# Kernel optimization log

Measured on AMD Instinct MI355X. Metric: run time of the kernel, lower is better.

## Reference

```python
import jax, jax.numpy as jnp
import numpy as np
from jax import lax

LATENT = 64
NUM_EMB = 512
BETA = 0.25
DN = ('NCHW', 'OIHW', 'NCHW')


def conv(x, w, b, stride, pad):
    y = lax.conv_general_dilated(x, w, (stride, stride), [(pad, pad), (pad, pad)],
                                 dimension_numbers=DN)
    return y + b[None, :, None, None]


def tconv(x, w, b, stride, pad, opad):
    # torch ConvTranspose2d(k=3, stride, padding=pad, output_padding=opad)
    # == dilated conv with lhs_dilation=stride, padding (k-1-pad, k-1-pad+opad),
    #    spatially-flipped kernel. w is stored OIHW (out, in, kh, kw).
    k = w.shape[2]
    lo, hi = k - 1 - pad, k - 1 - pad + opad
    y = lax.conv_general_dilated(x, w[:, :, ::-1, ::-1], (1, 1), [(lo, hi), (lo, hi)],
                                 lhs_dilation=(stride, stride), dimension_numbers=DN)
    return y + b[None, :, None, None]


def vector_quantize(z, codebook):
    # z: (B, D, H, W); codebook: (K, D)
    B, D, H, W = z.shape
    flat = z.transpose(0, 2, 3, 1).reshape(-1, D)  # (BHW, D)
    d = (jnp.sum(flat ** 2, axis=1, keepdims=True)
         + jnp.sum(codebook ** 2, axis=1)
         - 2.0 * flat @ codebook.T)  # (BHW, K)
    idx = jnp.argmin(d, axis=1)
    q = codebook[idx].reshape(B, H, W, D).transpose(0, 3, 1, 2)  # (B, D, H, W)
    commitment = jnp.mean((lax.stop_gradient(q) - z) ** 2)
    codebook_loss = jnp.mean((q - lax.stop_gradient(z)) ** 2)
    loss = BETA * commitment + codebook_loss
    q_ste = z + lax.stop_gradient(q - z)  # straight-through estimator
    return q_ste, loss


def setup_inputs() -> dict:
    key = jax.random.key(0)
    ks = jax.random.split(key, 16)
    f32 = jnp.float32
    inp = {
        'x': jax.random.uniform(ks[0], (1024, 1, 50, 50), dtype=f32),
        'enc_w1': jax.random.normal(ks[1], (32, 1, 3, 3), f32) * 0.1,
        'enc_b1': jnp.zeros((32,), f32),
        'enc_w2': jax.random.normal(ks[2], (64, 32, 3, 3), f32) * 0.05,
        'enc_b2': jnp.zeros((64,), f32),
        'enc_w3': jax.random.normal(ks[3], (LATENT, 64, 1, 1), f32) * 0.1,
        'enc_b3': jnp.zeros((LATENT,), f32),
        'codebook': jax.random.uniform(ks[4], (NUM_EMB, LATENT), dtype=f32),
        'dec_w1': jax.random.normal(ks[5], (64, LATENT, 3, 3), f32) * 0.05,
        'dec_b1': jnp.zeros((64,), f32),
        'dec_w2': jax.random.normal(ks[6], (32, 64, 3, 3), f32) * 0.05,
        'dec_b2': jnp.zeros((32,), f32),
        'dec_w3': jax.random.normal(ks[7], (1, 32, 3, 3), f32) * 0.05,
        'dec_b3': jnp.zeros((1,), f32),
    }
    return inp


def reference(x, enc_w1, enc_b1, enc_w2, enc_b2, enc_w3, enc_b3, codebook,
              dec_w1, dec_b1, dec_w2, dec_b2, dec_w3, dec_b3):
    # encoder: (B,1,50,50) -> (B,LATENT,13,13)
    h = jax.nn.relu(conv(x, enc_w1, enc_b1, 2, 1))
    h = jax.nn.relu(conv(h, enc_w2, enc_b2, 2, 1))
    z = conv(h, enc_w3, enc_b3, 1, 0)
    q, vq_loss = vector_quantize(z, codebook)
    # decoder: 13 -> 25 -> 50
    h = jax.nn.relu(tconv(q, dec_w1, dec_b1, 2, 1, 0))
    h = jax.nn.relu(tconv(h, dec_w2, dec_b2, 2, 1, 1))
    x_recon = jax.nn.sigmoid(conv(h, dec_w3, dec_b3, 1, 1))
    return x_recon, vq_loss
```

## Files before the change

kernel.cpp:

```cpp
#include <hip/hip_runtime.h>
#include <math.h>


typedef __attribute__((ext_vector_type(8))) short s8v;
typedef __attribute__((ext_vector_type(4))) float f4v;
typedef __attribute__((ext_vector_type(4))) int i4v;
typedef __attribute__((ext_vector_type(4))) short s4v;
typedef __attribute__((ext_vector_type(2))) float f2v;

__device__ inline unsigned short f2bf(float f) {
    unsigned u = __builtin_bit_cast(unsigned, f);
    return (unsigned short)((u + 0x7fffu + ((u >> 16) & 1u)) >> 16);
}
__device__ inline float bf2f(unsigned short h) {
    return __builtin_bit_cast(float, ((unsigned)h) << 16);
}

__global__ __launch_bounds__(256) void k_prep_all(
        const float* __restrict__ cb,  const float* __restrict__ ew2,
        const float* __restrict__ ew3, const float* __restrict__ dw1,
        const float* __restrict__ dw2, const float* __restrict__ dw3,
        unsigned short* __restrict__ cbm, unsigned short* __restrict__ wB2n,
        unsigned short* __restrict__ wB1, unsigned short* __restrict__ wB2,
        unsigned short* __restrict__ wB3, float* __restrict__ cn,
        float* __restrict__ loss, f2v* __restrict__ wpk) {
    int i = blockIdx.x * 256 + threadIdx.x;
    if (i < 98304) {
        int j = i & 7, lane = (i >> 3) & 63;
        int kc = (i >> 9) % 6, nt = (i >> 9) / 6;
        int n = nt * 16 + (lane & 15);
        int k = kc * 32 + ((lane >> 4) << 3) + j;
        int seg = k >> 6, kk = k & 63;
        float c = cb[n * 64 + kk];
        unsigned short ch = f2bf(c);
        cbm[i] = (seg == 1) ? f2bf(c - bf2f(ch)) : ch;
    } else if (i < 153600) {
        int q = i - 98304;
        int j = q & 7, lane = (q >> 3) & 63;
        int kc = (q >> 9) % 27, nt = (q >> 9) / 27;
        int k = kc * 32 + ((lane >> 4) << 3) + j;
        int co = nt * 16 + (lane & 15);
        int part = (k < 288) ? 0 : (k < 576) ? 1 : 0;
        int kk = (k < 288) ? k : (k < 576) ? k - 288 : k - 576;
        int tap = kk >> 5, ci = kk & 31;
        float v = ew2[(co * 32 + ci) * 9 + tap];
        unsigned short hi = f2bf(v);
        wB2n[q] = part ? f2bf(v - bf2f(hi)) : hi;
    } else if (i < 219136) {
        int q = i - 153600;
        int j = q & 7, l = (q >> 3) & 63, kc = (q >> 9) & 7, nt = q >> 12;
        int n = nt * 16 + (l & 15), k = kc * 32 + (l >> 4) * 8 + j;
        int cls = n >> 6, co = n & 63, p = k >> 6, ci = k & 63;
        int jh = -1, jw = -1;
        if (cls == 0)      { if (p == 0) { jh = 1; jw = 1; } }
        else if (cls == 1) { if (p == 1) { jh = 1; jw = 0; } else if (p == 0) { jh = 1; jw = 2; } }
        else if (cls == 2) { if (p == 2) { jh = 0; jw = 1; } else if (p == 0) { jh = 2; jw = 1; } }
        else { if (p == 3) { jh = 0; jw = 0; } else if (p == 2) { jh = 0; jw = 2; }
               else if (p == 1) { jh = 2; jw = 0; } else { jh = 2; jw = 2; } }
        float v = (jh >= 0) ? dw1[((co * 64 + ci) * 3 + jh) * 3 + jw] : 0.f;
        wB1[q] = f2bf(v);
    } else if (i < 251904) {
        int q = i - 219136;
        int j = q & 7, l = (q >> 3) & 63, kc = (q >> 9) & 7, nt = q >> 12;
        int n = nt * 16 + (l & 15), k = kc * 32 + (l >> 4) * 8 + j;
        int cls = n >> 5, co = n & 31, p = k >> 6, ci = k & 63;
        int jh = -1, jw = -1;
        if (cls == 0)      { if (p == 0) { jh = 1; jw = 1; } }
        else if (cls == 1) { if (p == 1) { jh = 1; jw = 0; } else if (p == 0) { jh = 1; jw = 2; } }
        else if (cls == 2) { if (p == 2) { jh = 0; jw = 1; } else if (p == 0) { jh = 2; jw = 1; } }
        else { if (p == 3) { jh = 0; jw = 0; } else if (p == 2) { jh = 0; jw = 2; }
               else if (p == 1) { jh = 2; jw = 0; } else { jh = 2; jw = 2; } }
        float v = (jh >= 0) ? dw2[((co * 64 + ci) * 3 + jh) * 3 + jw] : 0.f;
        wB2[q] = f2bf(v);
    } else if (i < 264192) {
        int q = i - 251904;
        int j = q & 7, lane = (q >> 3) & 63;
        int kc = (q >> 9) % 6, nt = (q >> 9) / 6;
        int k = kc * 32 + ((lane >> 4) << 3) + j;
        int n = nt * 16 + (lane & 15);
        int part = (k < 64) ? 0 : (k < 128) ? 1 : 0;
        int kk = (k < 64) ? k : (k < 128) ? k - 64 : k - 128;
        float v = ew3[n * 64 + kk];
        unsigned short hi = f2bf(v);
        wB3[q] = part ? f2bf(v - bf2f(hi)) : hi;
    } else if (i < 264704) {
        int k = i - 264192;
        const float* r = cb + k * 64;
        float s = 0.f;
#pragma unroll
        for (int c = 0; c < 64; ++c) s += r[c] * r[c];
        cn[k] = s;
    } else if (i == 264704) {
        *loss = 0.f;
    } else if (i < 264849) {
        int q = i - 264705;
        int kw = q / 48, rem = q % 48, kh = rem / 16, ii = rem % 16;
        f2v w;
        w[0] = dw3[(2 * ii) * 9 + kh * 3 + kw];
        w[1] = dw3[(2 * ii + 1) * 9 + kh * 3 + kw];
        wpk[q] = w;
    }
}

__global__ __launch_bounds__(256) void k_conv1(const float* __restrict__ x,
                                               const float* __restrict__ w,
                                               const float* __restrict__ b,
                                               unsigned short* __restrict__ h1,
                                               int total) {
    __shared__ float4 wl4[72];
    float* wl = (float*)wl4;
    int tid = threadIdx.x;
    for (int t = tid; t < 288; t += 256) {
        int tap = t >> 5, co = t & 31;
        wl[t] = w[co * 9 + tap];
    }
    __syncthreads();
    int pix = blockIdx.x * 256 + tid;
    if (pix >= total) return;
    int n = pix / 625, p = pix % 625, oh = p / 25, ow = p % 25;
    const float* xp = x + (size_t)n * 2500;
    float4 a[8];
#pragma unroll
    for (int j = 0; j < 8; ++j) a[j] = ((const float4*)b)[j];
#pragma unroll
    for (int kh = 0; kh < 3; ++kh) {
        int ih = 2 * oh - 1 + kh;
        if ((unsigned)ih >= 50u) continue;
#pragma unroll
        for (int kw = 0; kw < 3; ++kw) {
            int iw = 2 * ow - 1 + kw;
            if ((unsigned)iw >= 50u) continue;
            float v = xp[ih * 50 + iw];
            int tap = kh * 3 + kw;
#pragma unroll
            for (int j = 0; j < 8; ++j) {
                float4 ww = wl4[tap * 8 + j];
                a[j].x += v * ww.x; a[j].y += v * ww.y;
                a[j].z += v * ww.z; a[j].w += v * ww.w;
            }
        }
    }
    unsigned short hi[32], lo[32];
#pragma unroll
    for (int j = 0; j < 8; ++j) {
        float vv[4] = {a[j].x, a[j].y, a[j].z, a[j].w};
#pragma unroll
        for (int e = 0; e < 4; ++e) {
            float v = fmaxf(vv[e], 0.f);
            unsigned short h = f2bf(v);
            hi[j * 4 + e] = h;
            lo[j * 4 + e] = f2bf(v - bf2f(h));
        }
    }
    i4v* op = (i4v*)(h1 + (size_t)pix * 64);
#pragma unroll
    for (int g = 0; g < 4; ++g) {
        i4v ph, pl;
#pragma unroll
        for (int e = 0; e < 4; ++e) {
            int b0 = g * 8 + e * 2;
            ph[e] = (int)((unsigned)hi[b0] | ((unsigned)hi[b0 + 1] << 16));
            pl[e] = (int)((unsigned)lo[b0] | ((unsigned)lo[b0 + 1] << 16));
        }
        op[g] = ph;
        op[4 + g] = pl;
    }
}

__global__ __launch_bounds__(256) void k_enc_m(const unsigned short* __restrict__ h1,
                                               const unsigned short* __restrict__ B2n,
                                               const unsigned short* __restrict__ B3,
                                               const float* __restrict__ b2,
                                               const float* __restrict__ b3,
                                               unsigned short* __restrict__ z, int npix) {
    __shared__ short a1[16 * 872];
    __shared__ short a2[16 * 200];
    __shared__ short czs[16 * 136];
    int tid = threadIdx.x, blk = blockIdx.x;
    {
        int m = tid >> 4, chunk = tid & 15;
        if (chunk < 9) {
            int pix = blk * 16 + m;
            i4v vh[4], vl[4];
#pragma unroll
            for (int g = 0; g < 4; ++g) {
                vh[g] = (i4v){0, 0, 0, 0};
                vl[g] = (i4v){0, 0, 0, 0};
            }
            if (pix < npix) {
                int n = pix / 169, p = pix % 169, oh = p / 13, ow = p % 13;
                int kh = chunk / 3, kw = chunk % 3;
                int ih = 2 * oh - 1 + kh, iw = 2 * ow - 1 + kw;
                if (((unsigned)ih < 25u) && ((unsigned)iw < 25u)) {
                    const i4v* ip = (const i4v*)(h1 + (((size_t)n * 25 + ih) * 25 + iw) * 64);
#pragma unroll
                    for (int g = 0; g < 4; ++g) { vh[g] = ip[g]; vl[g] = ip[4 + g]; }
                }
            }
            short* row = a1 + m * 872 + chunk * 32;
            i4v* d0 = (i4v*)row;
            i4v* d1 = (i4v*)(row + 288);
            i4v* d2 = (i4v*)(row + 576);
#pragma unroll
            for (int g = 0; g < 4; ++g) { d0[g] = vh[g]; d1[g] = vh[g]; d2[g] = vl[g]; }
        }
    }
    __syncthreads();
    int wave = tid >> 6, lane = tid & 63;
    int arow1 = (lane & 15) * 872 + (lane >> 4) * 8;
    f4v acc = (f4v){0.f, 0.f, 0.f, 0.f};
#pragma unroll
    for (int kc = 0; kc < 27; ++kc) {
        s8v a = *(const s8v*)(a1 + arow1 + kc * 32);
        s8v b = *(const s8v*)((const short*)B2n + ((size_t)((wave * 27 + kc) * 64 + lane)) * 8);
        acc = __builtin_amdgcn_mfma_f32_16x16x32_bf16(a, b, acc, 0, 0, 0);
    }
    {
        float bv = b2[wave * 16 + (lane & 15)];
        int n = wave * 16 + (lane & 15);
#pragma unroll
        for (int r = 0; r < 4; ++r) {
            int m = (lane >> 4) * 4 + r;
            float h = fmaxf(acc[r] + bv, 0.f);
            unsigned short hh = f2bf(h);
            unsigned short ll = f2bf(h - bf2f(hh));
            a2[m * 200 + n] = (short)hh;
            a2[m * 200 + 64 + n] = (short)hh;
            a2[m * 200 + 128 + n] = (short)ll;
        }
    }
    __syncthreads();
    int arow2 = (lane & 15) * 200 + (lane >> 4) * 8;
    f4v acc2 = (f4v){0.f, 0.f, 0.f, 0.f};
#pragma unroll
    for (int kc = 0; kc < 6; ++kc) {
        s8v a = *(const s8v*)(a2 + arow2 + kc * 32);
        s8v b = *(const s8v*)((const short*)B3 + ((size_t)((wave * 6 + kc) * 64 + lane)) * 8);
        acc2 = __builtin_amdgcn_mfma_f32_16x16x32_bf16(a, b, acc2, 0, 0, 0);
    }
    {
        float bv = b3[wave * 16 + (lane & 15)];
        int n = wave * 16 + (lane & 15);
#pragma unroll
        for (int r = 0; r < 4; ++r) {
            int m = (lane >> 4) * 4 + r;
            float v = acc2[r] + bv;
            unsigned short hh = f2bf(v);
            czs[m * 136 + n] = (short)hh;
            czs[m * 136 + 64 + n] = (short)f2bf(v - bf2f(hh));
        }
    }
    __syncthreads();
    {
        int m = tid >> 4, t = tid & 15;
        int pix = blk * 16 + m;
        if (pix < npix)
            *(i4v*)(z + (size_t)pix * 128 + t * 8) = *(i4v*)(czs + m * 136 + t * 8);
    }
}

__global__ __launch_bounds__(256, 2) void k_vq_m(const unsigned short* __restrict__ z,
                                                 const float* __restrict__ cb,
                                                 const unsigned short* __restrict__ cbm,
                                                 const float* __restrict__ cn,
                                                 unsigned short* __restrict__ q,
                                                 float* __restrict__ lpart, int npix) {
    __shared__ short a_lds[128 * 136];
    __shared__ int bkf[128];
    __shared__ float lred4[4];
    int tid = threadIdx.x, blk = blockIdx.x;
    {
        const i4v* src = (const i4v*)(z + (size_t)blk * 128 * 128);
#pragma unroll
        for (int it = 0; it < 8; ++it) {
            int L = it * 256 + tid;
            int m = L >> 4, s = L & 15;
            int pix = blk * 128 + m;
            i4v v = (i4v){0, 0, 0, 0};
            if (pix < npix) v = src[L];
            *(i4v*)(a_lds + m * 136 + s * 8) = v;
        }
    }
    __syncthreads();
    int wave = tid >> 6, lane = tid & 63;
    int arow0 = (wave * 32 + (lane & 15)) * 136 + (lane >> 4) * 8;
    int arow1 = arow0 + 16 * 136;
    s8v af00 = *(const s8v*)(a_lds + arow0);
    s8v af01 = *(const s8v*)(a_lds + arow0 + 32);
    s8v af02 = *(const s8v*)(a_lds + arow0 + 64);
    s8v af03 = *(const s8v*)(a_lds + arow0 + 96);
    s8v af10 = *(const s8v*)(a_lds + arow1);
    s8v af11 = *(const s8v*)(a_lds + arow1 + 32);
    s8v af12 = *(const s8v*)(a_lds + arow1 + 64);
    s8v af13 = *(const s8v*)(a_lds + arow1 + 96);
    float bd0[4], bd1[4];
    int bk0[4], bk1[4];
#pragma unroll
    for (int r = 0; r < 4; ++r) {
        bd0[r] = 3.4e38f; bk0[r] = 0;
        bd1[r] = 3.4e38f; bk1[r] = 0;
    }
    const s8v* bp = (const s8v*)cbm + lane;
    int ln15 = lane & 15;
    s8v bfA[6], bfB[6];
#pragma unroll
    for (int kc = 0; kc < 6; ++kc) bfA[kc] = bp[kc * 64];
    float cnA = cn[ln15];
    float cnB;
    for (int nt = 0; nt < 32; nt += 2) {
#pragma unroll
        for (int kc = 0; kc < 6; ++kc) bfB[kc] = bp[((nt + 1) * 6 + kc) * 64];
        cnB = cn[(nt + 1) * 16 + ln15];
        {
            f4v acc0 = (f4v){0.f, 0.f, 0.f, 0.f};
            f4v acc1 = (f4v){0.f, 0.f, 0.f, 0.f};
            acc0 = __builtin_amdgcn_mfma_f32_16x16x32_bf16(af00, bfA[0], acc0, 0, 0, 0);
            acc1 = __builtin_amdgcn_mfma_f32_16x16x32_bf16(af10, bfA[0], acc1, 0, 0, 0);
            acc0 = __builtin_amdgcn_mfma_f32_16x16x32_bf16(af01, bfA[1], acc0, 0, 0, 0);
            acc1 = __builtin_amdgcn_mfma_f32_16x16x32_bf16(af11, bfA[1], acc1, 0, 0, 0);
            acc0 = __builtin_amdgcn_mfma_f32_16x16x32_bf16(af00, bfA[2], acc0, 0, 0, 0);
            acc1 = __builtin_amdgcn_mfma_f32_16x16x32_bf16(af10, bfA[2], acc1, 0, 0, 0);
            acc0 = __builtin_amdgcn_mfma_f32_16x16x32_bf16(af01, bfA[3], acc0, 0, 0, 0);
            acc1 = __builtin_amdgcn_mfma_f32_16x16x32_bf16(af11, bfA[3], acc1, 0, 0, 0);
            acc0 = __builtin_amdgcn_mfma_f32_16x16x32_bf16(af02, bfA[4], acc0, 0, 0, 0);
            acc1 = __builtin_amdgcn_mfma_f32_16x16x32_bf16(af12, bfA[4], acc1, 0, 0, 0);
            acc0 = __builtin_amdgcn_mfma_f32_16x16x32_bf16(af03, bfA[5], acc0, 0, 0, 0);
            acc1 = __builtin_amdgcn_mfma_f32_16x16x32_bf16(af13, bfA[5], acc1, 0, 0, 0);
            int kcol = nt * 16 + ln15;
#pragma unroll
            for (int r = 0; r < 4; ++r) {
                float d0 = cnA - 2.f * acc0[r];
                if (d0 < bd0[r]) { bd0[r] = d0; bk0[r] = kcol; }
                float d1 = cnA - 2.f * acc1[r];
                if (d1 < bd1[r]) { bd1[r] = d1; bk1[r] = kcol; }
            }
        }
        if (nt + 2 < 32) {
#pragma unroll
            for (int kc = 0; kc < 6; ++kc) bfA[kc] = bp[((nt + 2) * 6 + kc) * 64];
            cnA = cn[(nt + 2) * 16 + ln15];
        }
        {
            f4v acc0 = (f4v){0.f, 0.f, 0.f, 0.f};
            f4v acc1 = (f4v){0.f, 0.f, 0.f, 0.f};
            acc0 = __builtin_amdgcn_mfma_f32_16x16x32_bf16(af00, bfB[0], acc0, 0, 0, 0);
            acc1 = __builtin_amdgcn_mfma_f32_16x16x32_bf16(af10, bfB[0], acc1, 0, 0, 0);
            acc0 = __builtin_amdgcn_mfma_f32_16x16x32_bf16(af01, bfB[1], acc0, 0, 0, 0);
            acc1 = __builtin_amdgcn_mfma_f32_16x16x32_bf16(af11, bfB[1], acc1, 0, 0, 0);
            acc0 = __builtin_amdgcn_mfma_f32_16x16x32_bf16(af00, bfB[2], acc0, 0, 0, 0);
            acc1 = __builtin_amdgcn_mfma_f32_16x16x32_bf16(af10, bfB[2], acc1, 0, 0, 0);
            acc0 = __builtin_amdgcn_mfma_f32_16x16x32_bf16(af01, bfB[3], acc0, 0, 0, 0);
            acc1 = __builtin_amdgcn_mfma_f32_16x16x32_bf16(af11, bfB[3], acc1, 0, 0, 0);
            acc0 = __builtin_amdgcn_mfma_f32_16x16x32_bf16(af02, bfB[4], acc0, 0, 0, 0);
            acc1 = __builtin_amdgcn_mfma_f32_16x16x32_bf16(af12, bfB[4], acc1, 0, 0, 0);
            acc0 = __builtin_amdgcn_mfma_f32_16x16x32_bf16(af03, bfB[5], acc0, 0, 0, 0);
            acc1 = __builtin_amdgcn_mfma_f32_16x16x32_bf16(af13, bfB[5], acc1, 0, 0, 0);
            int kcol = (nt + 1) * 16 + ln15;
#pragma unroll
            for (int r = 0; r < 4; ++r) {
                float d0 = cnB - 2.f * acc0[r];
                if (d0 < bd0[r]) { bd0[r] = d0; bk0[r] = kcol; }
                float d1 = cnB - 2.f * acc1[r];
                if (d1 < bd1[r]) { bd1[r] = d1; bk1[r] = kcol; }
            }
        }
    }
#pragma unroll
    for (int off = 1; off < 16; off <<= 1) {
#pragma unroll
        for (int r = 0; r < 4; ++r) {
            float od = __shfl_xor(bd0[r], off);
            int ok = __shfl_xor(bk0[r], off);
            if (od < bd0[r] || (od == bd0[r] && ok < bk0[r])) { bd0[r] = od; bk0[r] = ok; }
            od = __shfl_xor(bd1[r], off);
            ok = __shfl_xor(bk1[r], off);
            if (od < bd1[r] || (od == bd1[r] && ok < bk1[r])) { bd1[r] = od; bk1[r] = ok; }
        }
    }
    if ((lane & 15) == 0) {
#pragma unroll
        for (int r = 0; r < 4; ++r) {
            bkf[wave * 32 + (lane >> 4) * 4 + r] = bk0[r];
            bkf[wave * 32 + 16 + (lane >> 4) * 4 + r] = bk1[r];
        }
    }
    __syncthreads();
    float lsum = 0.f;
#pragma unroll
    for (int it = 0; it < 8; ++it) {
        int L = it * 256 + tid;
        int m = L >> 4, c4 = L & 15;
        int pix = blk * 128 + m;
        if (pix < npix) {
            int k0 = bkf[m];
            float4 cq = ((const float4*)cb)[(size_t)k0 * 16 + c4];
            const short* rz = a_lds + m * 136 + c4 * 4;
            s4v zh4 = *(const s4v*)rz;
            s4v zl4 = *(const s4v*)(rz + 64);
            float zx = bf2f((unsigned short)zh4[0]) + bf2f((unsigned short)zl4[0]);
            float zy = bf2f((unsigned short)zh4[1]) + bf2f((unsigned short)zl4[1]);
            float zz = bf2f((unsigned short)zh4[2]) + bf2f((unsigned short)zl4[2]);
            float zw = bf2f((unsigned short)zh4[3]) + bf2f((unsigned short)zl4[3]);
            float dx = cq.x - zx, dy = cq.y - zy, dz = cq.z - zz, dw = cq.w - zw;
            lsum += dx * dx + dy * dy + dz * dz + dw * dw;
            s4v qs;
            qs[0] = (short)f2bf(cq.x); qs[1] = (short)f2bf(cq.y);
            qs[2] = (short)f2bf(cq.z); qs[3] = (short)f2bf(cq.w);
            *(s4v*)(q + (size_t)pix * 64 + c4 * 4) = qs;
        }
    }
#pragma unroll
    for (int off = 32; off > 0; off >>= 1) lsum += __shfl_down(lsum, off);
    if (lane == 0) lred4[wave] = lsum;
    __syncthreads();
    if (tid == 0) lpart[blk] = lred4[0] + lred4[1] + lred4[2] + lred4[3];
}

__global__ __launch_bounds__(256) void k_loss(const float* __restrict__ lpart,
                                              int nblk, float* __restrict__ loss) {
    int tid = threadIdx.x;
    float s = 0.f;
    for (int i = tid; i < nblk; i += 256) s += lpart[i];
#pragma unroll
    for (int off = 32; off > 0; off >>= 1) s += __shfl_down(s, off);
    __shared__ float w4[4];
    if ((tid & 63) == 0) w4[tid >> 6] = s;
    __syncthreads();
    if (tid == 0)
        atomicAdd(loss, (w4[0] + w4[1] + w4[2] + w4[3]) * (1.25f / 11075584.f));
}

__global__ __launch_bounds__(256) void k_tconv1_m(const unsigned short* __restrict__ q,
                                                  const unsigned short* __restrict__ wB,
                                                  const float* __restrict__ bias,
                                                  unsigned short* __restrict__ d1,
                                                  int nquad) {
    __shared__ short a_lds[32 * 264];
    __shared__ short c_lds[32 * 264];
    int tid = threadIdx.x, blk = blockIdx.x;
#pragma unroll
    for (int pass = 0; pass < 4; ++pass) {
        int idx = tid + pass * 256;
        int m = idx >> 5, sub = idx & 31;
        int qg = blk * 32 + m;
        int p = sub >> 3, ci0 = (sub & 7) * 8;
        i4v v = (i4v){0, 0, 0, 0};
        if (qg < nquad) {
            int img = qg / 169, r = qg % 169, qm = r / 13, qw = r % 13;
            int sm = qm + (p >> 1), sw = qw + (p & 1);
            if (sm < 13 && sw < 13)
                v = *(const i4v*)(q + (((size_t)img * 13 + sm) * 13 + sw) * 64 + ci0);
        }
        *(i4v*)(a_lds + m * 264 + sub * 8) = v;
    }
    __syncthreads();
    int wave = tid >> 6, lane = tid & 63;
    f4v acc[2][4];
#pragma unroll
    for (int mt = 0; mt < 2; ++mt)
#pragma unroll
        for (int i = 0; i < 4; ++i) acc[mt][i] = (f4v){0.f, 0.f, 0.f, 0.f};
    float bv[4];
#pragma unroll
    for (int i = 0; i < 4; ++i) bv[i] = bias[((wave * 4 + i) * 16 + (lane & 15)) & 63];
#pragma unroll
    for (int kc = 0; kc < 8; ++kc) {
        s8v a0 = *(const s8v*)(a_lds + ((lane & 15)) * 264 + (lane >> 4) * 8 + kc * 32);
        s8v a1 = *(const s8v*)(a_lds + (16 + (lane & 15)) * 264 + (lane >> 4) * 8 + kc * 32);
#pragma unroll
        for (int i = 0; i < 4; ++i) {
            int nt = wave * 4 + i;
            s8v b = *(const s8v*)((const short*)wB + ((size_t)((nt * 8 + kc) * 64 + lane)) * 8);
            acc[0][i] = __builtin_amdgcn_mfma_f32_16x16x32_bf16(a0, b, acc[0][i], 0, 0, 0);
            acc[1][i] = __builtin_amdgcn_mfma_f32_16x16x32_bf16(a1, b, acc[1][i], 0, 0, 0);
        }
    }
#pragma unroll
    for (int mt = 0; mt < 2; ++mt)
#pragma unroll
        for (int i = 0; i < 4; ++i) {
            int n = (wave * 4 + i) * 16 + (lane & 15);
#pragma unroll
            for (int r2 = 0; r2 < 4; ++r2) {
                int m = mt * 16 + (lane >> 4) * 4 + r2;
                float v = fmaxf(acc[mt][i][r2] + bv[i], 0.f);
                c_lds[m * 264 + n] = (short)f2bf(v);
            }
        }
    __syncthreads();
#pragma unroll
    for (int pass = 0; pass < 4; ++pass) {
        int ch = tid + pass * 256;
        int m = ch >> 5, cpart = ch & 31;
        int qg = blk * 32 + m;
        if (qg >= nquad) continue;
        int img = qg / 169, r = qg % 169, qm = r / 13, qw = r % 13;
        int cls = cpart >> 3, co8 = (cpart & 7) * 8;
        int oh = 2 * qm + (cls >> 1), ow = 2 * qw + (cls & 1);
        if (oh >= 25 || ow >= 25) continue;
        i4v val = *(i4v*)(c_lds + m * 264 + cls * 64 + co8);
        *(i4v*)(d1 + (((size_t)img * 25 + oh) * 25 + ow) * 64 + co8) = val;
    }
}

__global__ __launch_bounds__(256) void k_tconv2_m(const unsigned short* __restrict__ d1,
                                                  const unsigned short* __restrict__ wB,
                                                  const float* __restrict__ bias,
                                                  unsigned short* __restrict__ d2,
                                                  int nquad) {
    __shared__ short a_lds[32 * 264];
    __shared__ short c_lds[32 * 136];
    int tid = threadIdx.x, blk = blockIdx.x;
#pragma unroll
    for (int pass = 0; pass < 4; ++pass) {
        int idx = tid + pass * 256;
        int m = idx >> 5, sub = idx & 31;
        int qg = blk * 32 + m;
        int p = sub >> 3, ci0 = (sub & 7) * 8;
        i4v v = (i4v){0, 0, 0, 0};
        if (qg < nquad) {
            int img = qg / 625, r = qg % 625, qm = r / 25, qw = r % 25;
            int sm = qm + (p >> 1), sw = qw + (p & 1);
            if (sm < 25 && sw < 25)
                v = *(const i4v*)(d1 + (((size_t)img * 25 + sm) * 25 + sw) * 64 + ci0);
        }
        *(i4v*)(a_lds + m * 264 + sub * 8) = v;
    }
    __syncthreads();
    int wave = tid >> 6, lane = tid & 63;
    f4v acc[2][2];
#pragma unroll
    for (int mt = 0; mt < 2; ++mt)
#pragma unroll
        for (int i = 0; i < 2; ++i) acc[mt][i] = (f4v){0.f, 0.f, 0.f, 0.f};
    float bv[2];
#pragma unroll
    for (int i = 0; i < 2; ++i) bv[i] = bias[((wave * 2 + i) * 16 + (lane & 15)) & 31];
#pragma unroll
    for (int kc = 0; kc < 8; ++kc) {
        s8v a0 = *(const s8v*)(a_lds + ((lane & 15)) * 264 + (lane >> 4) * 8 + kc * 32);
        s8v a1 = *(const s8v*)(a_lds + (16 + (lane & 15)) * 264 + (lane >> 4) * 8 + kc * 32);
#pragma unroll
        for (int i = 0; i < 2; ++i) {
            int nt = wave * 2 + i;
            s8v b = *(const s8v*)((const short*)wB + ((size_t)((nt * 8 + kc) * 64 + lane)) * 8);
            acc[0][i] = __builtin_amdgcn_mfma_f32_16x16x32_bf16(a0, b, acc[0][i], 0, 0, 0);
            acc[1][i] = __builtin_amdgcn_mfma_f32_16x16x32_bf16(a1, b, acc[1][i], 0, 0, 0);
        }
    }
#pragma unroll
    for (int mt = 0; mt < 2; ++mt)
#pragma unroll
        for (int i = 0; i < 2; ++i) {
            int n = (wave * 2 + i) * 16 + (lane & 15);
#pragma unroll
            for (int r2 = 0; r2 < 4; ++r2) {
                int m = mt * 16 + (lane >> 4) * 4 + r2;
                float v = fmaxf(acc[mt][i][r2] + bv[i], 0.f);
                c_lds[m * 136 + n] = (short)f2bf(v);
            }
        }
    __syncthreads();
#pragma unroll
    for (int pass = 0; pass < 2; ++pass) {
        int ch = tid + pass * 256;
        int m = ch >> 4, cpart = ch & 15;
        int qg = blk * 32 + m;
        if (qg >= nquad) continue;
        int img = qg / 625, r = qg % 625, qm = r / 25, qw = r % 25;
        int cls = cpart >> 2, co8 = (cpart & 3) * 8;
        int oh = 2 * qm + (cls >> 1), ow = 2 * qw + (cls & 1);
        i4v val = *(i4v*)(c_lds + m * 136 + cls * 32 + co8);
        *(i4v*)(d2 + (((size_t)img * 50 + oh) * 50 + ow) * 32 + co8) = val;
    }
}

__global__ __launch_bounds__(256, 2) void k_convf(const unsigned short* __restrict__ in,
                                                  const f2v* __restrict__ wpk,
                                                  const float* __restrict__ b,
                                                  float* __restrict__ out, int nthr) {
    int t = blockIdx.x * 256 + threadIdx.x;
    if (t >= nthr) return;
    int img = t / 250, r = t % 250;
    int strip = r / 50, col = r % 50;
    int r0 = strip * 10;
    const unsigned short* base = in + (size_t)img * 80000;
    f2v acc[10];
#pragma unroll
    for (int i = 0; i < 10; ++i) acc[i] = (f2v){0.f, 0.f};
    for (int dx = -1; dx <= 1; ++dx) {
        int ic = col + dx;
        if ((unsigned)ic >= 50u) continue;
        int kw = dx + 1;
        const f2v* wp = wpk + kw * 48;
        f2v w2r[3][16];
#pragma unroll
        for (int kh = 0; kh < 3; ++kh)
#pragma unroll
            for (int i = 0; i < 16; ++i) w2r[kh][i] = wp[kh * 16 + i];
#pragma unroll
        for (int rr = -1; rr <= 10; ++rr) {
            int ih = r0 + rr;
            if ((unsigned)ih >= 50u) continue;
            const i4v* px = (const i4v*)(base + ((size_t)ih * 50 + ic) * 32);
#pragma unroll
            for (int c8 = 0; c8 < 4; ++c8) {
                i4v u = px[c8];
#pragma unroll
                for (int e = 0; e < 4; ++e) {
                    unsigned uu = (unsigned)u[e];
                    f2v x;
                    x[0] = __builtin_bit_cast(float, uu << 16);
                    x[1] = __builtin_bit_cast(float, uu & 0xffff0000u);
                    int i = c8 * 4 + e;
                    if (rr - 1 >= 0 && rr - 1 <= 9) acc[rr - 1] += x * w2r[2][i];
                    if (rr >= 0 && rr <= 9)         acc[rr]     += x * w2r[1][i];
                    if (rr + 1 >= 0 && rr + 1 <= 9) acc[rr + 1] += x * w2r[0][i];
                }
            }
        }
    }
    float b0 = b[0];
    float* op = out + (size_t)img * 2500 + (size_t)r0 * 50 + col;
#pragma unroll
    for (int i = 0; i < 10; ++i) {
        float v = acc[i][0] + acc[i][1] + b0;
        op[(size_t)i * 50] = 1.f / (1.f + expf(-v));
    }
}

extern "C" void kernel_launch(void* const* d_in, const int* in_sizes, int n_in,
                              void* d_out, int out_size, void* d_ws, size_t ws_size,
                              hipStream_t stream) {
    const float* x   = (const float*)d_in[0];
    const float* ew1 = (const float*)d_in[1];
    const float* eb1 = (const float*)d_in[2];
    const float* ew2 = (const float*)d_in[3];
    const float* eb2 = (const float*)d_in[4];
    const float* ew3 = (const float*)d_in[5];
    const float* eb3 = (const float*)d_in[6];
    const float* cb  = (const float*)d_in[7];
    const float* dw1 = (const float*)d_in[8];
    const float* db1 = (const float*)d_in[9];
    const float* dw2 = (const float*)d_in[10];
    const float* db2 = (const float*)d_in[11];
    const float* dw3 = (const float*)d_in[12];
    const float* db3 = (const float*)d_in[13];
    float* out = (float*)d_out;
    float* loss = out + 2560000;

    float* ws = (float*)d_ws;
    float* cn = ws;
    unsigned short* wB1  = (unsigned short*)(ws + 512);
    unsigned short* wB2  = (unsigned short*)(ws + 33280);
    unsigned short* wB2n = (unsigned short*)(ws + 49664);
    unsigned short* wB3  = (unsigned short*)(ws + 77312);
    unsigned short* cbm  = (unsigned short*)(ws + 83456);
    float* lpart = ws + 132608;
    f2v* wpk = (f2v*)(ws + 133968);
    const size_t tw_floats = 134256;

    const int B = 1024;
    const size_t A_per = 40000, B_per = 20000;
    size_t avail = (ws_size / 4 > tw_floats) ? ws_size / 4 - tw_floats : 0;
    int BC = (int)(avail / (A_per + B_per));
    if (BC > B) BC = B;
    if (BC < 1) BC = 1;
    float* regA = ws + tw_floats;
    float* regB = regA + (size_t)BC * A_per;

    k_prep_all<<<1035, 256, 0, stream>>>(cb, ew2, ew3, dw1, dw2, dw3,
                                         cbm, wB2n, wB1, wB2, wB3, cn, loss, wpk);

    for (int n0 = 0; n0 < B; n0 += BC) {
        int bc = (B - n0 < BC) ? (B - n0) : BC;
        const float* xch = x + (size_t)n0 * 2500;

        int t1 = bc * 625;
        unsigned short* h1p = (unsigned short*)regA;
        k_conv1<<<(t1 + 255) / 256, 256, 0, stream>>>(xch, ew1, eb1, h1p, t1);

        int npix = bc * 169;
        unsigned short* zp = (unsigned short*)regB;
        k_enc_m<<<(npix + 15) / 16, 256, 0, stream>>>(h1p, wB2n, wB3, eb2, eb3, zp, npix);

        unsigned short* qb = (unsigned short*)regA;
        int nblk = (npix + 127) / 128;
        k_vq_m<<<nblk, 256, 0, stream>>>(zp, cb, cbm, cn, qb, lpart, npix);

        k_loss<<<1, 256, 0, stream>>>(lpart, nblk, loss);

        unsigned short* d1 = (unsigned short*)regB;
        k_tconv1_m<<<(npix + 31) / 32, 256, 0, stream>>>(qb, wB1, db1, d1, npix);

        int nq2 = bc * 625;
        unsigned short* d2 = (unsigned short*)regA;
        k_tconv2_m<<<(nq2 + 31) / 32, 256, 0, stream>>>(d1, wB2, db2, d2, nq2);

        int t6 = bc * 250;
        k_convf<<<(t6 + 255) / 256, 256, 0, stream>>>(d2, wpk, db3, out + (size_t)n0 * 2500, t6);
    }
}
```

Measured before the change: 452.1 us.

## Tile transposed convolutions by image row pairs and gather im2col from shared tiles

New measurement: 442.8 us. 2.0% less time.

```diff
diff --git a/kernel.cpp b/kernel.cpp
--- a/kernel.cpp
+++ b/kernel.cpp
@@ -430,31 +430,36 @@
         atomicAdd(loss, (w4[0] + w4[1] + w4[2] + w4[3]) * (1.25f / 11075584.f));
 }
 
-__global__ __launch_bounds__(256) void k_tconv1_m(const unsigned short* __restrict__ q,
-                                                  const unsigned short* __restrict__ wB,
-                                                  const float* __restrict__ bias,
-                                                  unsigned short* __restrict__ d1,
-                                                  int nquad) {
-    __shared__ short a_lds[32 * 264];
+__global__ __launch_bounds__(256, 4) void k_tconv1_m(const unsigned short* __restrict__ q,
+                                                     const unsigned short* __restrict__ wB,
+                                                     const float* __restrict__ bias,
+                                                     unsigned short* __restrict__ d1) {
+    __shared__ short a_t[3 * 14 * 72];
     __shared__ short c_lds[32 * 264];
-    int tid = threadIdx.x, blk = blockIdx.x;
-#pragma unroll
-    for (int pass = 0; pass < 4; ++pass) {
-        int idx = tid + pass * 256;
-        int m = idx >> 5, sub = idx & 31;
-        int qg = blk * 32 + m;
-        int p = sub >> 3, ci0 = (sub & 7) * 8;
-        i4v v = (i4v){0, 0, 0, 0};
-        if (qg < nquad) {
-            int img = qg / 169, r = qg % 169, qm = r / 13, qw = r % 13;
-            int sm = qm + (p >> 1), sw = qw + (p & 1);
-            if (sm < 13 && sw < 13)
-                v = *(const i4v*)(q + (((size_t)img * 13 + sm) * 13 + sw) * 64 + ci0);
-        }
-        *(i4v*)(a_lds + m * 264 + sub * 8) = v;
+    int tid = threadIdx.x;
+    int b = blockIdx.x, img = blockIdx.y;
+#pragma unroll
+    for (int pass = 0; pass < 2; ++pass) {
+        int u = tid + pass * 256;
+        if (u < 384) {
+            int px = u >> 3, part = u & 7;
+            int r = px >> 4, c = px & 15;
+            if (c < 14) {
+                i4v v = (i4v){0, 0, 0, 0};
+                int grow = 2 * b + r;
+                if (grow < 13 && c < 13)
+                    v = *(const i4v*)(q + ((size_t)img * 169 + grow * 13 + c) * 64 + part * 8);
+                *(i4v*)(a_t + (r * 14 + c) * 72 + part * 8) = v;
+            }
+        }
     }
     __syncthreads();
     int wave = tid >> 6, lane = tid & 63;
+    int g8 = (lane >> 4) * 8;
+    int qw = lane & 15;
+    int qwc = (qw < 13) ? qw : 0;
+    int base0 = qwc * 72;
+    int base1 = (14 + qwc) * 72;
     f4v acc[2][4];
 #pragma unroll
     for (int mt = 0; mt < 2; ++mt)
@@ -465,14 +470,17 @@
     for (int i = 0; i < 4; ++i) bv[i] = bias[((wave * 4 + i) * 16 + (lane & 15)) & 63];
 #pragma unroll
     for (int kc = 0; kc < 8; ++kc) {
-        s8v a0 = *(const s8v*)(a_lds + ((lane & 15)) * 264 + (lane >> 4) * 8 + kc * 32);
-        s8v a1 = *(const s8v*)(a_lds + (16 + (lane & 15)) * 264 + (lane >> 4) * 8 + kc * 32);
+        int k0 = kc * 32 + g8;
+        int p = k0 >> 6, ci0 = k0 & 63;
+        int off = ((p >> 1) * 14 + (p & 1)) * 72 + ci0;
+        s8v a0 = *(const s8v*)(a_t + base0 + off);
+        s8v a1 = *(const s8v*)(a_t + base1 + off);
 #pragma unroll
         for (int i = 0; i < 4; ++i) {
             int nt = wave * 4 + i;
-            s8v b = *(const s8v*)((const short*)wB + ((size_t)((nt * 8 + kc) * 64 + lane)) * 8);
-            acc[0][i] = __builtin_amdgcn_mfma_f32_16x16x32_bf16(a0, b, acc[0][i], 0, 0, 0);
-            acc[1][i] = __builtin_amdgcn_mfma_f32_16x16x32_bf16(a1, b, acc[1][i], 0, 0, 0);
+            s8v bb = *(const s8v*)((const short*)wB + ((size_t)((nt * 8 + kc) * 64 + lane)) * 8);
+            acc[0][i] = __builtin_amdgcn_mfma_f32_16x16x32_bf16(a0, bb, acc[0][i], 0, 0, 0);
+            acc[1][i] = __builtin_amdgcn_mfma_f32_16x16x32_bf16(a1, bb, acc[1][i], 0, 0, 0);
         }
     }
 #pragma unroll
@@ -492,45 +500,52 @@
     for (int pass = 0; pass < 4; ++pass) {
         int ch = tid + pass * 256;
         int m = ch >> 5, cpart = ch & 31;
-        int qg = blk * 32 + m;
-        if (qg >= nquad) continue;
-        int img = qg / 169, r = qg % 169, qm = r / 13, qw = r % 13;
+        int qwO = m & 15, qr = m >> 4;
+        if (qwO >= 13) continue;
+        int qm = 2 * b + qr;
+        if (qm >= 13) continue;
         int cls = cpart >> 3, co8 = (cpart & 7) * 8;
-        int oh = 2 * qm + (cls >> 1), ow = 2 * qw + (cls & 1);
+        int oh = 2 * qm + (cls >> 1), ow = 2 * qwO + (cls & 1);
         if (oh >= 25 || ow >= 25) continue;
         i4v val = *(i4v*)(c_lds + m * 264 + cls * 64 + co8);
         *(i4v*)(d1 + (((size_t)img * 25 + oh) * 25 + ow) * 64 + co8) = val;
     }
 }
 
-__global__ __launch_bounds__(256) void k_tconv2_m(const unsigned short* __restrict__ d1,
-                                                  const unsigned short* __restrict__ wB,
-                                                  const float* __restrict__ bias,
-                                                  unsigned short* __restrict__ d2,
-                                                  int nquad) {
-    __shared__ short a_lds[32 * 264];
-    __shared__ short c_lds[32 * 136];
-    int tid = threadIdx.x, blk = blockIdx.x;
-#pragma unroll
-    for (int pass = 0; pass < 4; ++pass) {
-        int idx = tid + pass * 256;
-        int m = idx >> 5, sub = idx & 31;
-        int qg = blk * 32 + m;
-        int p = sub >> 3, ci0 = (sub & 7) * 8;
-        i4v v = (i4v){0, 0, 0, 0};
-        if (qg < nquad) {
-            int img = qg / 625, r = qg % 625, qm = r / 25, qw = r % 25;
-            int sm = qm + (p >> 1), sw = qw + (p & 1);
-            if (sm < 25 && sw < 25)
-                v = *(const i4v*)(d1 + (((size_t)img * 25 + sm) * 25 + sw) * 64 + ci0);
-        }
-        *(i4v*)(a_lds + m * 264 + sub * 8) = v;
+__global__ __launch_bounds__(256, 4) void k_tconv2_m(const unsigned short* __restrict__ d1,
+                                                     const unsigned short* __restrict__ wB,
+                                                     const float* __restrict__ bias,
+                                                     unsigned short* __restrict__ d2) {
+    __shared__ short a_t[3 * 26 * 72];
+    __shared__ short c_lds[64 * 136];
+    int tid = threadIdx.x;
+    int b = blockIdx.x, img = blockIdx.y;
+#pragma unroll
+    for (int pass = 0; pass < 3; ++pass) {
+        int u = tid + pass * 256;
+        int px = u >> 3, part = u & 7;
+        int r = px >> 5, c = px & 31;
+        if (c < 26) {
+            i4v v = (i4v){0, 0, 0, 0};
+            int grow = 2 * b + r;
+            if (grow < 25 && c < 25)
+                v = *(const i4v*)(d1 + (((size_t)img * 25 + grow) * 25 + c) * 64 + part * 8);
+            *(i4v*)(a_t + (r * 26 + c) * 72 + part * 8) = v;
+        }
     }
     __syncthreads();
     int wave = tid >> 6, lane = tid & 63;
-    f4v acc[2][2];
-#pragma unroll
-    for (int mt = 0; mt < 2; ++mt)
+    int g8 = (lane >> 4) * 8;
+    int qwA = lane & 15;
+    int qwB = 16 + (lane & 15);
+    int qBc = (qwB < 25) ? qwB : 0;
+    int base0 = qwA * 72;
+    int base1 = qBc * 72;
+    int base2 = (26 + qwA) * 72;
+    int base3 = (26 + qBc) * 72;
+    f4v acc[4][2];
+#pragma unroll
+    for (int mt = 0; mt < 4; ++mt)
 #pragma unroll
         for (int i = 0; i < 2; ++i) acc[mt][i] = (f4v){0.f, 0.f, 0.f, 0.f};
     float bv[2];
@@ -538,18 +553,25 @@
     for (int i = 0; i < 2; ++i) bv[i] = bias[((wave * 2 + i) * 16 + (lane & 15)) & 31];
 #pragma unroll
     for (int kc = 0; kc < 8; ++kc) {
-        s8v a0 = *(const s8v*)(a_lds + ((lane & 15)) * 264 + (lane >> 4) * 8 + kc * 32);
-        s8v a1 = *(const s8v*)(a_lds + (16 + (lane & 15)) * 264 + (lane >> 4) * 8 + kc * 32);
+        int k0 = kc * 32 + g8;
+        int p = k0 >> 6, ci0 = k0 & 63;
+        int off = ((p >> 1) * 26 + (p & 1)) * 72 + ci0;
+        s8v a0 = *(const s8v*)(a_t + base0 + off);
+        s8v a1 = *(const s8v*)(a_t + base1 + off);
+        s8v a2 = *(const s8v*)(a_t + base2 + off);
+        s8v a3 = *(const s8v*)(a_t + base3 + off);
 #pragma unroll
         for (int i = 0; i < 2; ++i) {
             int nt = wave * 2 + i;
-            s8v b = *(const s8v*)((const short*)wB + ((size_t)((nt * 8 + kc) * 64 + lane)) * 8);
-            acc[0][i] = __builtin_amdgcn_mfma_f32_16x16x32_bf16(a0, b, acc[0][i], 0, 0, 0);
-            acc[1][i] = __builtin_amdgcn_mfma_f32_16x16x32_bf16(a1, b, acc[1][i], 0, 0, 0);
-        }
-    }
-#pragma unroll
-    for (int mt = 0; mt < 2; ++mt)
+            s8v bb = *(const s8v*)((const short*)wB + ((size_t)((nt * 8 + kc) * 64 + lane)) * 8);
+            acc[0][i] = __builtin_amdgcn_mfma_f32_16x16x32_bf16(a0, bb, acc[0][i], 0, 0, 0);
+            acc[1][i] = __builtin_amdgcn_mfma_f32_16x16x32_bf16(a1, bb, acc[1][i], 0, 0, 0);
+            acc[2][i] = __builtin_amdgcn_mfma_f32_16x16x32_bf16(a2, bb, acc[2][i], 0, 0, 0);
+            acc[3][i] = __builtin_amdgcn_mfma_f32_16x16x32_bf16(a3, bb, acc[3][i], 0, 0, 0);
+        }
+    }
+#pragma unroll
+    for (int mt = 0; mt < 4; ++mt)
 #pragma unroll
         for (int i = 0; i < 2; ++i) {
             int n = (wave * 2 + i) * 16 + (lane & 15);
@@ -562,14 +584,15 @@
         }
     __syncthreads();
 #pragma unroll
-    for (int pass = 0; pass < 2; ++pass) {
+    for (int pass = 0; pass < 4; ++pass) {
         int ch = tid + pass * 256;
         int m = ch >> 4, cpart = ch & 15;
-        int qg = blk * 32 + m;
-        if (qg >= nquad) continue;
-        int img = qg / 625, r = qg % 625, qm = r / 25, qw = r % 25;
+        int qwO = m & 31, qr = m >> 5;
+        if (qwO >= 25) continue;
+        int qm = 2 * b + qr;
+        if (qm >= 25) continue;
         int cls = cpart >> 2, co8 = (cpart & 3) * 8;
-        int oh = 2 * qm + (cls >> 1), ow = 2 * qw + (cls & 1);
+        int oh = 2 * qm + (cls >> 1), ow = 2 * qwO + (cls & 1);
         i4v val = *(i4v*)(c_lds + m * 136 + cls * 32 + co8);
         *(i4v*)(d2 + (((size_t)img * 50 + oh) * 50 + ow) * 32 + co8) = val;
     }
@@ -691,11 +714,10 @@
         k_loss<<<1, 256, 0, stream>>>(lpart, nblk, loss);
 
         unsigned short* d1 = (unsigned short*)regB;
-        k_tconv1_m<<<(npix + 31) / 32, 256, 0, stream>>>(qb, wB1, db1, d1, npix);
-
-        int nq2 = bc * 625;
+        k_tconv1_m<<<dim3(7, bc), 256, 0, stream>>>(qb, wB1, db1, d1);
+
         unsigned short* d2 = (unsigned short*)regA;
-        k_tconv2_m<<<(nq2 + 31) / 32, 256, 0, stream>>>(d1, wB2, db2, d2, nq2);
+        k_tconv2_m<<<dim3(13, bc), 256, 0, stream>>>(d1, wB2, db2, d2);
 
         int t6 = bc * 250;
         k_convf<<<(t6 + 255) / 256, 256, 0, stream>>>(d2, wpk, db3, out + (size_t)n0 * 2500, t6);
```
